# Optimization experiments

Measured on AMD Instinct MI355X. Metric: run time of the kernel, lower is better.

The kernel has to match this reference:

```python
import jax, jax.numpy as jnp
import numpy as np

C, HEADS, K, P, S = 384, 12, 3, 1, 1
B, H, W = 8, 56, 56


def _unfold(v, k, p, s):
    # v: [B, C, Hs, Ws] -> [B, C, k*k, oh*ow], matching torch.nn.Unfold layout
    b, c, hs, ws = v.shape
    vp = jnp.pad(v, ((0, 0), (0, 0), (p, p), (p, p)))
    oh = (hs + 2 * p - k) // s + 1
    ow = (ws + 2 * p - k) // s + 1
    patches = jnp.stack(
        [vp[:, :, i:i + oh * s:s, j:j + ow * s:s] for i in range(k) for j in range(k)],
        axis=2,
    )  # [B, C, k*k, oh, ow]
    return patches.reshape(b, c, k * k, oh * ow)


def _fold(patches, out_h, out_w, k, p, s):
    # patches: [B, C, k*k, oh, ow] -> scatter-add to [B, C, out_h, out_w]
    b, c, _, oh, ow = patches.shape
    out = jnp.zeros((b, c, out_h + 2 * p, out_w + 2 * p), patches.dtype)
    for i in range(k):
        for j in range(k):
            out = out.at[:, :, i:i + oh * s:s, j:j + ow * s:s].add(patches[:, :, i * k + j])
    return out[:, :, p:p + out_h, p:p + out_w]


def setup_inputs() -> dict:
    key = jax.random.key(0)
    ks = jax.random.split(key, 6)
    sc = C ** -0.5
    return {
        "x": jax.random.normal(ks[0], (B, C, H, W), jnp.float32),
        "Wv": jax.random.normal(ks[1], (C, C), jnp.float32) * sc,
        "Wa": jax.random.normal(ks[2], (K ** 4 * HEADS, C), jnp.float32) * sc,
        "ba": jax.random.normal(ks[3], (K ** 4 * HEADS,), jnp.float32) * 0.01,
        "Wp": jax.random.normal(ks[4], (C, C), jnp.float32) * sc,
        "bp": jax.random.normal(ks[5], (C,), jnp.float32) * 0.01,
    }


def reference(x, Wv, Wa, ba, Wp, bp):
    b, c, h, w = x.shape
    hd = c // HEADS
    height = -(-h // S)
    width = -(-w // S)
    L = height * width
    x_hwc = x.transpose(0, 2, 3, 1)  # [B,H,W,C]
    # value projection, then the original's spatial transpose quirk: [B,C,W,H]
    v = jnp.einsum('bhwc,dc->bdwh', x_hwc, Wv)
    v = _unfold(v, K, P, S)  # [B, C, k*k, L]
    v = v.reshape(b, HEADS, hd, K * K, L).transpose(0, 1, 4, 3, 2)  # [B,n,L,k2,hd]
    # avgPool with kernel=stride=1 is identity
    a = jnp.einsum('bhwc,ec->bhwe', x_hwc, Wa) + ba
    a = a.reshape(b, L, HEADS, K * K, K * K).transpose(0, 2, 1, 3, 4)
    a = jax.nn.softmax(a * (hd ** -0.5), axis=-1)  # [B,n,L,k2,k2]
    out = jnp.einsum('bnlpq,bnlqd->bnlpd', a, v)  # [B,n,L,k2,hd]
    out = out.transpose(0, 1, 4, 3, 2).reshape(b, c, K * K, height, width)
    out = _fold(out, h, w, K, P, S)  # [B,C,H,W]
    out = jnp.einsum('bchw,dc->bhwd', out, Wp) + bp
    return out.transpose(0, 3, 1, 2)
```

## Files before the change

kernel.cpp:

```cpp
#include <hip/hip_runtime.h>
#include <hip/hip_bf16.h>
#include <math.h>

#define BATCH 8
#define CIN   384
#define HEADS 12
#define HGT   56
#define WID   56
#define HW    3136
#define NPIX  (BATCH*HW)
#define NVAL  384
#define NATT_W 1152
#define NQKV  1536
#define KSTEPS (CIN/32)
#define MB_TOT 196

typedef __bf16 bf16x8 __attribute__((ext_vector_type(8)));
typedef __bf16 bf16x4 __attribute__((ext_vector_type(4)));
typedef float f32x4 __attribute__((ext_vector_type(4)));
typedef __hip_bfloat16 hbf16;

__device__ __forceinline__ void gload_lds16(const void* g, void* l) {
  __builtin_amdgcn_global_load_lds(
      (const __attribute__((address_space(1))) void*)g,
      (__attribute__((address_space(3))) void*)l, 16, 0, 0);
}

#define NB_CONVX 9408
#define NB_WQKV  2304
#define NB_WP    576
__global__ __launch_bounds__(256) void prep_all(
    const float* __restrict__ x,
    const float* __restrict__ Wv, const float* __restrict__ Wa,
    const float* __restrict__ ba, const float* __restrict__ Wp,
    hbf16* __restrict__ xb, hbf16* __restrict__ wcat,
    float* __restrict__ bcat, hbf16* __restrict__ wpb)
{
  const int bid = blockIdx.x;
  const int tid = threadIdx.x;
  if (bid < NB_CONVX) {
    __shared__ float s[32][33];
    const int xt = bid % 98;
    const int yt = (bid / 98) % 12;
    const int b  = bid / (98 * 12);
    const int hw0 = xt * 32, c0 = yt * 32;
    const int tx = tid & 31, ty = tid >> 5;
    #pragma unroll
    for (int i = 0; i < 4; i++) {
      int c = c0 + ty + i * 8;
      s[ty + i * 8][tx] = x[((size_t)b * CIN + c) * HW + hw0 + tx];
    }
    __syncthreads();
    #pragma unroll
    for (int i = 0; i < 4; i++) {
      int hw = hw0 + ty + i * 8;
      xb[((size_t)b * HW + hw) * CIN + c0 + tx] =
          __float2bfloat16(s[tx][ty + i * 8]);
    }
  } else if (bid < NB_CONVX + NB_WQKV) {
    const int i = (bid - NB_CONVX) * 256 + tid;
    if (i < NQKV * CIN) {
      int n = i / CIN, k = i % CIN;
      float v = 0.f;
      if (n < NVAL) {
        v = Wv[(size_t)n * CIN + k];
      } else {
        int a = n - NVAL;
        int head = a / 96, r = a % 96, p = r / 10, q = r % 10;
        if (p < 9 && q < 9)
          v = Wa[(size_t)(head * 81 + p * 9 + q) * CIN + k];
      }
      wcat[i] = __float2bfloat16(v);
    }
    if (i < NQKV) {
      float bv = 0.f;
      if (i >= NVAL) {
        int a = i - NVAL;
        int head = a / 96, r = a % 96, p = r / 10, q = r % 10;
        if (p < 9 && q < 9) bv = ba[head * 81 + p * 9 + q];
      }
      bcat[i] = bv;
    }
  } else {
    const int i = (bid - NB_CONVX - NB_WQKV) * 256 + tid;
    if (i < CIN * CIN) wpb[i] = __float2bfloat16(Wp[i]);
  }
}

template<int MODE>
__global__ __launch_bounds__(256, 4) void gemm_fused(
    const hbf16* __restrict__ A_,
    const hbf16* __restrict__ Bt_,
    const float* __restrict__ bias,
    hbf16* __restrict__ ovp,
    hbf16* __restrict__ oat,
    float* __restrict__ oput)
{
  __shared__ __align__(16) char smem[33280];
  const __bf16* A  = (const __bf16*)A_;
  const __bf16* Bt = (const __bf16*)Bt_;

  const int tid  = threadIdx.x;
  const int wave = tid >> 6, lane = tid & 63;
  const int wr = wave >> 1, wc = wave & 1;
  const int l16 = lane & 15, kg = lane >> 4;

  const int NBN   = (MODE == 0) ? (NQKV / 128) : (NVAL / 128);
  const int FULLB = 8 * NBN * (MB_TOT / 8);
  int mb, nb;
  {
    const int wgid = blockIdx.x;
    if (wgid < FULLB) {
      const int xc = wgid & 7, r = wgid >> 3;
      nb = r % NBN;
      mb = (r / NBN) * 8 + xc;
    } else {
      const int l = wgid - FULLB;
      nb = l >> 2;
      mb = (MB_TOT & ~7) + (l & 3);
    }
  }
  const int m0 = mb * 128, n0 = nb * 128;

  float* biasLds = (float*)(smem + 32768);
  if (tid < 128) biasLds[tid] = bias[n0 + tid];

  const int srow = tid >> 2;
  const int skb  = (tid & 3) * 16;

  f32x4 acc[4][4] = {};

  auto stage = [&](int k0, int buf) {
    const char* gA = (const char*)(A  + (size_t)m0 * CIN + k0);
    const char* gB = (const char*)(Bt + (size_t)n0 * CIN + k0);
    char* lA = smem + buf * 16384;
    char* lB = smem + buf * 16384 + 8192;
    #pragma unroll
    for (int p = 0; p < 2; p++) {
      int row = p * 64 + srow;
      gload_lds16(gA + (size_t)row * (CIN * 2) + skb, lA + p * 4096 + wave * 1024);
      gload_lds16(gB + (size_t)row * (CIN * 2) + skb, lB + p * 4096 + wave * 1024);
    }
  };

  stage(0, 0);
  __syncthreads();

  for (int t = 0; t < KSTEPS; ++t) {
    const int buf = t & 1;
    if (t + 1 < KSTEPS) stage((t + 1) * 32, buf ^ 1);

    const __bf16* As = (const __bf16*)(smem + buf * 16384);
    const __bf16* Bs = (const __bf16*)(smem + buf * 16384 + 8192);
    bf16x8 af[4], bfr[4];
    #pragma unroll
    for (int mi = 0; mi < 4; mi++)
      af[mi] = *(const bf16x8*)(As + (wr * 64 + mi * 16 + l16) * 32 + kg * 8);
    #pragma unroll
    for (int ni = 0; ni < 4; ni++)
      bfr[ni] = *(const bf16x8*)(Bs + (wc * 64 + ni * 16 + l16) * 32 + kg * 8);
    #pragma unroll
    for (int mi = 0; mi < 4; mi++)
      #pragma unroll
      for (int ni = 0; ni < 4; ni++) {
        if (MODE == 0)
          acc[ni][mi] = __builtin_amdgcn_mfma_f32_16x16x32_bf16(
              bfr[ni], af[mi], acc[ni][mi], 0, 0, 0);
        else
          acc[mi][ni] = __builtin_amdgcn_mfma_f32_16x16x32_bf16(
              af[mi], bfr[ni], acc[mi][ni], 0, 0, 0);
      }
    __syncthreads();
  }

  if (MODE == 0) {
    __bf16* epi = (__bf16*)smem;
    #pragma unroll
    for (int ni = 0; ni < 4; ni++) {
      #pragma unroll
      for (int mi = 0; mi < 4; mi++) {
        const int m  = wr * 64 + mi * 16 + l16;
        const int nb2 = wc * 64 + ni * 16 + kg * 4;
        bf16x4 v4;
        #pragma unroll
        for (int r = 0; r < 4; r++)
          v4[r] = (__bf16)__float2bfloat16(acc[ni][mi][r] + biasLds[nb2 + r]);
        *(bf16x4*)(epi + m * 128 + (nb2 ^ ((m & 7) << 3))) = v4;
      }
    }
    __syncthreads();
    const bool isv = (n0 < NVAL);
    #pragma unroll
    for (int q = 0; q < 8; q++) {
      const int cid = q * 256 + tid;
      const int m = cid >> 4, nc = cid & 15;
      const int nloc = nc * 8;
      bf16x8 v = *(const bf16x8*)(epi + m * 128 + (nloc ^ ((m & 7) << 3)));
      const int mg = m0 + m;
      if (isv)
        *(bf16x8*)(ovp + (size_t)mg * NVAL + n0 + nloc) = v;
      else
        *(bf16x8*)(oat + (size_t)mg * NATT_W + (n0 - NVAL) + nloc) = v;
    }
  } else {
    float* epi = (float*)smem;
    #pragma unroll
    for (int p = 0; p < 2; p++) {
      if (p) __syncthreads();
      if (wr == p) {
        #pragma unroll
        for (int mi = 0; mi < 4; mi++) {
          #pragma unroll
          for (int ni = 0; ni < 4; ni++) {
            const int n  = wc * 64 + ni * 16 + l16;
            const int ml = mi * 16 + kg * 4;
            f32x4 v;
            #pragma unroll
            for (int r = 0; r < 4; r++) v[r] = acc[mi][ni][r] + biasLds[n];
            *(f32x4*)(epi + n * 64 + (ml ^ ((n & 7) << 2))) = v;
          }
        }
      }
      __syncthreads();
      #pragma unroll
      for (int q = 0; q < 8; q++) {
        const int cid = q * 256 + tid;
        const int n = cid >> 4, mc = cid & 15;
        const int ml = mc * 4;
        f32x4 v = *(const f32x4*)(epi + n * 64 + (ml ^ ((n & 7) << 2)));
        const int mg = m0 + p * 64 + ml;
        const int b = mg / HW, hw = mg % HW;
        *(f32x4*)(oput + ((size_t)b * NVAL + n0 + n) * HW + hw) = v;
      }
    }
  }
}

__global__ __launch_bounds__(256) void fold_fused(
    const hbf16* __restrict__ attnb,
    const hbf16* __restrict__ vprojb,
    hbf16* __restrict__ foldedb)
{
  __shared__ float Wl[16 * HEADS * 25];

  const int b    = blockIdx.x & 7;
  const int tile = blockIdx.x >> 3;
  const int tx = tile % 14, ty = tile / 14;
  const int x0 = tx * 4, y0 = ty * 4;
  const int bofs = b * HW;
  const int tid = threadIdx.x;
  const bool interior = (tx >= 1) && (tx <= 12) && (ty >= 1) && (ty <= 12);
  const float scale = 0.17677669529663687f;

  if (tid < 192) {
    const int pixL = tid / HEADS, head = tid - pixL * HEADS;
    const int y = y0 + (pixL >> 2), x = x0 + (pixL & 3);

    float W[25];
    #pragma unroll
    for (int k = 0; k < 25; k++) W[k] = 0.f;

    auto docenter = [&](int i, int j) {
      const uint32_t* rp = (const uint32_t*)(attnb +
          (size_t)(bofs + (y - i + 1) * WID + (x - j + 1)) * NATT_W +
          head * 96 + (i * 3 + j) * 10);
      float v[9];
      #pragma unroll
      for (int u = 0; u < 4; u++) {
        uint32_t bits = rp[u];
        v[2 * u]     = __uint_as_float(bits << 16) * scale;
        v[2 * u + 1] = __uint_as_float(bits & 0xffff0000u) * scale;
      }
      v[8] = __uint_as_float(rp[4] << 16) * scale;
      float m = -1e30f;
      #pragma unroll
      for (int q = 0; q < 9; q++) m = fmaxf(m, v[q]);
      float s = 0.f;
      #pragma unroll
      for (int q = 0; q < 9; q++) { v[q] = __expf(v[q] - m); s += v[q]; }
      const float inv = 1.f / s;
      #pragma unroll
      for (int ip = 0; ip < 3; ip++)
        #pragma unroll
        for (int jp = 0; jp < 3; jp++)
          W[(ip - i + 2) * 5 + (jp - j + 2)] += v[ip * 3 + jp] * inv;
    };

    if (interior) {
      #pragma unroll
      for (int i = 0; i < 3; i++)
        #pragma unroll
        for (int j = 0; j < 3; j++)
          docenter(i, j);
    } else {
      #pragma unroll
      for (int i = 0; i < 3; i++)
        #pragma unroll
        for (int j = 0; j < 3; j++) {
          const int hh = y - i + 1, ww = x - j + 1;
          if (hh >= 0 && hh < HGT && ww >= 0 && ww < WID) docenter(i, j);
        }
    }
    float* o = &Wl[tid * 25];
    #pragma unroll
    for (int k = 0; k < 25; k++) o[k] = W[k];
  }
  __syncthreads();

  const int pixL = tid >> 4;
  const int ch16 = tid & 15;
  const int y = y0 + (pixL >> 2), x = x0 + (pixL & 3);
  const size_t pixofs = (size_t)(bofs + y * WID + x);
  const hbf16* vb0 = vprojb + (size_t)(bofs + (x - 2) * WID + (y - 2)) * NVAL;

  #pragma unroll
  for (int it = 0; it < 3; it++) {
    const int c0 = ch16 * 8 + it * 128;
    const int head = c0 >> 5;
    const float* Wp = &Wl[(pixL * HEADS + head) * 25];
    float acc[8];
    #pragma unroll
    for (int k = 0; k < 8; k++) acc[k] = 0.f;

    if (interior) {
      #pragma unroll
      for (int a = 0; a < 5; a++)
        #pragma unroll
        for (int e = 0; e < 5; e++) {
          const float w_ = Wp[a * 5 + e];
          const uint32_t* v = (const uint32_t*)(vb0 + (e * WID + a) * NVAL + c0);
          uint32_t b0 = v[0], b1 = v[1], b2 = v[2], b3 = v[3];
          acc[0] += w_ * __uint_as_float(b0 << 16);
          acc[1] += w_ * __uint_as_float(b0 & 0xffff0000u);
          acc[2] += w_ * __uint_as_float(b1 << 16);
          acc[3] += w_ * __uint_as_float(b1 & 0xffff0000u);
          acc[4] += w_ * __uint_as_float(b2 << 16);
          acc[5] += w_ * __uint_as_float(b2 & 0xffff0000u);
          acc[6] += w_ * __uint_as_float(b3 << 16);
          acc[7] += w_ * __uint_as_float(b3 & 0xffff0000u);
        }
    } else {
      #pragma unroll
      for (int a = 0; a < 5; a++) {
        const int wi = y + a - 2;
        #pragma unroll
        for (int e = 0; e < 5; e++) {
          const int hi = x + e - 2;
          if (wi >= 0 && wi < WID && hi >= 0 && hi < HGT) {
            const float w_ = Wp[a * 5 + e];
            const uint32_t* v = (const uint32_t*)(
                vprojb + (size_t)(bofs + hi * WID + wi) * NVAL + c0);
            uint32_t b0 = v[0], b1 = v[1], b2 = v[2], b3 = v[3];
            acc[0] += w_ * __uint_as_float(b0 << 16);
            acc[1] += w_ * __uint_as_float(b0 & 0xffff0000u);
            acc[2] += w_ * __uint_as_float(b1 << 16);
            acc[3] += w_ * __uint_as_float(b1 & 0xffff0000u);
            acc[4] += w_ * __uint_as_float(b2 << 16);
            acc[5] += w_ * __uint_as_float(b2 & 0xffff0000u);
            acc[6] += w_ * __uint_as_float(b3 << 16);
            acc[7] += w_ * __uint_as_float(b3 & 0xffff0000u);
          }
        }
      }
    }

    bf16x8 o;
    #pragma unroll
    for (int k = 0; k < 8; k++) o[k] = (__bf16)__float2bfloat16(acc[k]);
    *(bf16x8*)(foldedb + pixofs * NVAL + c0) = o;
  }
}

extern "C" void kernel_launch(void* const* d_in, const int* in_sizes, int n_in,
                              void* d_out, int out_size, void* d_ws, size_t ws_size,
                              hipStream_t stream)
{
  const float* x  = (const float*)d_in[0];
  const float* Wv = (const float*)d_in[1];
  const float* Wa = (const float*)d_in[2];
  const float* ba = (const float*)d_in[3];
  const float* Wp = (const float*)d_in[4];
  const float* bp = (const float*)d_in[5];
  float* out = (float*)d_out;

  char* w = (char*)d_ws;
  const size_t ATTN_B  = (size_t)NPIX * NATT_W * 2;
  const size_t VPROJ_B = (size_t)NPIX * NVAL * 2;
  const size_t XB_B    = (size_t)NPIX * CIN * 2;
  hbf16* attnb  = (hbf16*)w;
  hbf16* vprojb = (hbf16*)(w + ATTN_B);
  hbf16* xb     = (hbf16*)(w + ATTN_B + VPROJ_B);
  hbf16* wcat   = (hbf16*)(w + ATTN_B + VPROJ_B + XB_B);
  hbf16* wpb    = wcat + (size_t)NQKV * CIN;
  float* bcat   = (float*)(wpb + (size_t)CIN * CIN);
  hbf16* foldedb = xb;

  prep_all<<<dim3(NB_CONVX + NB_WQKV + NB_WP), 256, 0, stream>>>(
      x, Wv, Wa, ba, Wp, xb, wcat, bcat, wpb);
  gemm_fused<0><<<dim3(MB_TOT * (NQKV / 128)), 256, 0, stream>>>(
      xb, wcat, bcat, vprojb, attnb, nullptr);
  fold_fused<<<dim3(8 * 196), 256, 0, stream>>>(attnb, vprojb, foldedb);
  gemm_fused<1><<<dim3(MB_TOT * (NVAL / 128)), 256, 0, stream>>>(
      foldedb, wpb, bp, nullptr, nullptr, out);
}
```

Before: 121.6 us.

## Fuse softmax into attention GEMM epilogue and scatter normalized weights to centers

Splits the QKV GEMM into a value-projection GEMM and a separate per-head attention GEMM with 96-wide N tiles whose epilogue performs the 9-way softmax and writes normalized weights scattered to the neighbor-center pixel layout. The fold kernel then reads one contiguous 192-byte row per (pixel, head) instead of nine strided gathers, and no longer recomputes softmax for each of the nine overlapping neighbors. This removes the ninefold redundant exp/normalize work and the gather traffic in fold. In exchange it adds an extra kernel launch, N tiles with partial B loads (96 of 128 rows), uncoalesced 4-byte scattered stores in the attention epilogue, and a new block-to-tile mapping that launches some idle blocks.

Measured after the change: 143.3 us. +17.9%, slower.

```diff
diff --git a/kernel.cpp b/kernel.cpp
--- a/kernel.cpp
+++ b/kernel.cpp
@@ -11,13 +11,14 @@
 #define NPIX  (BATCH*HW)
 #define NVAL  384
 #define NATT_W 1152
-#define NQKV  1536
 #define KSTEPS (CIN/32)
 #define MB_TOT 196
+#define NQKV  1536
 
 typedef __bf16 bf16x8 __attribute__((ext_vector_type(8)));
 typedef __bf16 bf16x4 __attribute__((ext_vector_type(4)));
 typedef float f32x4 __attribute__((ext_vector_type(4)));
+typedef uint32_t u32x4 __attribute__((ext_vector_type(4)));
 typedef __hip_bfloat16 hbf16;
 
 __device__ __forceinline__ void gload_lds16(const void* g, void* l) {
@@ -93,9 +94,14 @@
     const hbf16* __restrict__ Bt_,
     const float* __restrict__ bias,
     hbf16* __restrict__ ovp,
-    hbf16* __restrict__ oat,
     float* __restrict__ oput)
 {
+  const int xcd = blockIdx.x & 7;
+  const int idx = blockIdx.x >> 3;
+  const int mb = xcd * 25 + idx / 3;
+  const int nb = idx % 3;
+  if (mb >= MB_TOT) return;
+
   __shared__ __align__(16) char smem[33280];
   const __bf16* A  = (const __bf16*)A_;
   const __bf16* Bt = (const __bf16*)Bt_;
@@ -104,22 +110,6 @@
   const int wave = tid >> 6, lane = tid & 63;
   const int wr = wave >> 1, wc = wave & 1;
   const int l16 = lane & 15, kg = lane >> 4;
-
-  const int NBN   = (MODE == 0) ? (NQKV / 128) : (NVAL / 128);
-  const int FULLB = 8 * NBN * (MB_TOT / 8);
-  int mb, nb;
-  {
-    const int wgid = blockIdx.x;
-    if (wgid < FULLB) {
-      const int xc = wgid & 7, r = wgid >> 3;
-      nb = r % NBN;
-      mb = (r / NBN) * 8 + xc;
-    } else {
-      const int l = wgid - FULLB;
-      nb = l >> 2;
-      mb = (MB_TOT & ~7) + (l & 3);
-    }
-  }
   const int m0 = mb * 128, n0 = nb * 128;
 
   float* biasLds = (float*)(smem + 32768);
@@ -189,18 +179,13 @@
       }
     }
     __syncthreads();
-    const bool isv = (n0 < NVAL);
     #pragma unroll
     for (int q = 0; q < 8; q++) {
       const int cid = q * 256 + tid;
       const int m = cid >> 4, nc = cid & 15;
       const int nloc = nc * 8;
       bf16x8 v = *(const bf16x8*)(epi + m * 128 + (nloc ^ ((m & 7) << 3)));
-      const int mg = m0 + m;
-      if (isv)
-        *(bf16x8*)(ovp + (size_t)mg * NVAL + n0 + nloc) = v;
-      else
-        *(bf16x8*)(oat + (size_t)mg * NATT_W + (n0 - NVAL) + nloc) = v;
+      *(bf16x8*)(ovp + (size_t)(m0 + m) * NVAL + n0 + nloc) = v;
     }
   } else {
     float* epi = (float*)smem;
@@ -236,8 +221,142 @@
   }
 }
 
+__global__ __launch_bounds__(256, 4) void gemm_attn(
+    const hbf16* __restrict__ A_,
+    const hbf16* __restrict__ Bt_,
+    const float* __restrict__ bias,
+    hbf16* __restrict__ attn2)
+{
+  const int xcd = blockIdx.x & 7;
+  const int idx = blockIdx.x >> 3;
+  const int mb = xcd * 25 + idx / 12;
+  const int h  = idx % 12;
+  if (mb >= MB_TOT) return;
+
+  __shared__ __align__(16) char smem[33280];
+  const __bf16* A  = (const __bf16*)A_;
+  const __bf16* Bt = (const __bf16*)Bt_;
+
+  const int tid  = threadIdx.x;
+  const int wave = tid >> 6, lane = tid & 63;
+  const int wr = wave >> 1, wc = wave & 1;
+  const int l16 = lane & 15, kg = lane >> 4;
+  const int m0 = mb * 128;
+  const int n0w = NVAL + h * 96;
+
+  float* biasLds = (float*)(smem + 32768);
+  if (tid < 96) biasLds[tid] = bias[n0w + tid];
+
+  const int srow = tid >> 2;
+  const int skb  = (tid & 3) * 16;
+
+  f32x4 acc[3][4] = {};
+
+  auto stage = [&](int k0, int buf) {
+    const char* gA = (const char*)(A  + (size_t)m0 * CIN + k0);
+    const char* gB = (const char*)(Bt + (size_t)n0w * CIN + k0);
+    char* lA = smem + buf * 16384;
+    char* lB = smem + buf * 16384 + 8192;
+    #pragma unroll
+    for (int p = 0; p < 2; p++) {
+      int row = p * 64 + srow;
+      gload_lds16(gA + (size_t)row * (CIN * 2) + skb, lA + p * 4096 + wave * 1024);
+      if (row < 96)
+        gload_lds16(gB + (size_t)row * (CIN * 2) + skb, lB + p * 4096 + wave * 1024);
+    }
+  };
+
+  stage(0, 0);
+  __syncthreads();
+
+  for (int t = 0; t < KSTEPS; ++t) {
+    const int buf = t & 1;
+    if (t + 1 < KSTEPS) stage((t + 1) * 32, buf ^ 1);
+
+    const __bf16* As = (const __bf16*)(smem + buf * 16384);
+    const __bf16* Bs = (const __bf16*)(smem + buf * 16384 + 8192);
+    bf16x8 af[4], bfr[3];
+    #pragma unroll
+    for (int mi = 0; mi < 4; mi++)
+      af[mi] = *(const bf16x8*)(As + (wr * 64 + mi * 16 + l16) * 32 + kg * 8);
+    #pragma unroll
+    for (int ni = 0; ni < 3; ni++)
+      bfr[ni] = *(const bf16x8*)(Bs + (wc * 48 + ni * 16 + l16) * 32 + kg * 8);
+    #pragma unroll
+    for (int mi = 0; mi < 4; mi++)
+      #pragma unroll
+      for (int ni = 0; ni < 3; ni++)
+        acc[ni][mi] = __builtin_amdgcn_mfma_f32_16x16x32_bf16(
+            bfr[ni], af[mi], acc[ni][mi], 0, 0, 0);
+    __syncthreads();
+  }
+
+  __bf16* epi = (__bf16*)smem;
+  #pragma unroll
+  for (int ni = 0; ni < 3; ni++) {
+    #pragma unroll
+    for (int mi = 0; mi < 4; mi++) {
+      const int m  = wr * 64 + mi * 16 + l16;
+      const int nbse = wc * 48 + ni * 16 + kg * 4;
+      bf16x4 v4;
+      #pragma unroll
+      for (int r = 0; r < 4; r++)
+        v4[r] = (__bf16)__float2bfloat16(acc[ni][mi][r] + biasLds[nbse + r]);
+      *(bf16x4*)(epi + m * 100 + nbse) = v4;
+    }
+  }
+  __syncthreads();
+
+  const float scale = 0.17677669529663687f;
+  #pragma unroll
+  for (int it = 0; it < 5; it++) {
+    const int u = it * 256 + tid;
+    if (u < 1152) {
+      const int m = u & 127, p = u >> 7;
+      const uint32_t* rp = (const uint32_t*)(epi + m * 100 + p * 10);
+      float v[9];
+      #pragma unroll
+      for (int t2 = 0; t2 < 4; t2++) {
+        uint32_t bits = rp[t2];
+        v[2 * t2]     = __uint_as_float(bits << 16) * scale;
+        v[2 * t2 + 1] = __uint_as_float(bits & 0xffff0000u) * scale;
+      }
+      v[8] = __uint_as_float(rp[4] << 16) * scale;
+      float mx = -1e30f;
+      #pragma unroll
+      for (int q = 0; q < 9; q++) mx = fmaxf(mx, v[q]);
+      float s = 0.f;
+      #pragma unroll
+      for (int q = 0; q < 9; q++) { v[q] = __expf(v[q] - mx); s += v[q]; }
+      const float inv = 1.f / s;
+      #pragma unroll
+      for (int q = 0; q < 9; q++) v[q] *= inv;
+
+      const int mg = m0 + m;
+      const int b = mg / HW, yx = mg % HW;
+      const int y = yx / WID, x = yx % WID;
+      const int i = p / 3, j = p % 3;
+      const int yC = y + i - 1, xC = x + j - 1;
+      if ((unsigned)yC < HGT && (unsigned)xC < WID) {
+        uint32_t* dst = (uint32_t*)(attn2 +
+            (size_t)(b * HW + yC * WID + xC) * NATT_W + h * 96 + p * 10);
+        union { __bf16 hh[2]; uint32_t u32; } pk;
+        #pragma unroll
+        for (int k = 0; k < 4; k++) {
+          pk.hh[0] = (__bf16)__float2bfloat16(v[2 * k]);
+          pk.hh[1] = (__bf16)__float2bfloat16(v[2 * k + 1]);
+          dst[k] = pk.u32;
+        }
+        pk.hh[0] = (__bf16)__float2bfloat16(v[8]);
+        pk.hh[1] = (__bf16)0.f;
+        dst[4] = pk.u32;
+      }
+    }
+  }
+}
+
 __global__ __launch_bounds__(256) void fold_fused(
-    const hbf16* __restrict__ attnb,
+    const hbf16* __restrict__ attn2,
     const hbf16* __restrict__ vprojb,
     hbf16* __restrict__ foldedb)
 {
@@ -250,56 +369,45 @@
   const int bofs = b * HW;
   const int tid = threadIdx.x;
   const bool interior = (tx >= 1) && (tx <= 12) && (ty >= 1) && (ty <= 12);
-  const float scale = 0.17677669529663687f;
 
   if (tid < 192) {
     const int pixL = tid / HEADS, head = tid - pixL * HEADS;
     const int y = y0 + (pixL >> 2), x = x0 + (pixL & 3);
 
+    const u32x4* base = (const u32x4*)(attn2 +
+        (size_t)(bofs + y * WID + x) * NATT_W + head * 96);
+    u32x4 dv[12];
+    #pragma unroll
+    for (int k = 0; k < 12; k++) dv[k] = base[k];
+
     float W[25];
     #pragma unroll
     for (int k = 0; k < 25; k++) W[k] = 0.f;
 
-    auto docenter = [&](int i, int j) {
-      const uint32_t* rp = (const uint32_t*)(attnb +
-          (size_t)(bofs + (y - i + 1) * WID + (x - j + 1)) * NATT_W +
-          head * 96 + (i * 3 + j) * 10);
+    #pragma unroll
+    for (int r = 0; r < 9; r++) {
+      const int i = r / 3, j = r % 3;
+      if (!interior) {
+        const int hh = y - i + 1, ww = x - j + 1;
+        if (!((unsigned)hh < HGT && (unsigned)ww < WID)) continue;
+      }
       float v[9];
       #pragma unroll
-      for (int u = 0; u < 4; u++) {
-        uint32_t bits = rp[u];
-        v[2 * u]     = __uint_as_float(bits << 16) * scale;
-        v[2 * u + 1] = __uint_as_float(bits & 0xffff0000u) * scale;
-      }
-      v[8] = __uint_as_float(rp[4] << 16) * scale;
-      float m = -1e30f;
-      #pragma unroll
-      for (int q = 0; q < 9; q++) m = fmaxf(m, v[q]);
-      float s = 0.f;
-      #pragma unroll
-      for (int q = 0; q < 9; q++) { v[q] = __expf(v[q] - m); s += v[q]; }
-      const float inv = 1.f / s;
+      for (int t = 0; t < 4; t++) {
+        const int k = 5 * r + t;
+        const uint32_t bits = dv[k >> 2][k & 3];
+        v[2 * t]     = __uint_as_float(bits << 16);
+        v[2 * t + 1] = __uint_as_float(bits & 0xffff0000u);
+      }
+      {
+        const int k = 5 * r + 4;
+        v[8] = __uint_as_float(dv[k >> 2][k & 3] << 16);
+      }
       #pragma unroll
       for (int ip = 0; ip < 3; ip++)
         #pragma unroll
         for (int jp = 0; jp < 3; jp++)
-          W[(ip - i + 2) * 5 + (jp - j + 2)] += v[ip * 3 + jp] * inv;
-    };
-
-    if (interior) {
-      #pragma unroll
-      for (int i = 0; i < 3; i++)
-        #pragma unroll
-        for (int j = 0; j < 3; j++)
-          docenter(i, j);
-    } else {
-      #pragma unroll
-      for (int i = 0; i < 3; i++)
-        #pragma unroll
-        for (int j = 0; j < 3; j++) {
-          const int hh = y - i + 1, ww = x - j + 1;
-          if (hh >= 0 && hh < HGT && ww >= 0 && ww < WID) docenter(i, j);
-        }
+          W[(ip - i + 2) * 5 + (jp - j + 2)] += v[ip * 3 + jp];
     }
     float* o = &Wl[tid * 25];
     #pragma unroll
@@ -387,7 +495,7 @@
   const size_t ATTN_B  = (size_t)NPIX * NATT_W * 2;
   const size_t VPROJ_B = (size_t)NPIX * NVAL * 2;
   const size_t XB_B    = (size_t)NPIX * CIN * 2;
-  hbf16* attnb  = (hbf16*)w;
+  hbf16* attn2  = (hbf16*)w;
   hbf16* vprojb = (hbf16*)(w + ATTN_B);
   hbf16* xb     = (hbf16*)(w + ATTN_B + VPROJ_B);
   hbf16* wcat   = (hbf16*)(w + ATTN_B + VPROJ_B + XB_B);
@@ -397,9 +505,8 @@
 
   prep_all<<<dim3(NB_CONVX + NB_WQKV + NB_WP), 256, 0, stream>>>(
       x, Wv, Wa, ba, Wp, xb, wcat, bcat, wpb);
-  gemm_fused<0><<<dim3(MB_TOT * (NQKV / 128)), 256, 0, stream>>>(
-      xb, wcat, bcat, vprojb, attnb, nullptr);
-  fold_fused<<<dim3(8 * 196), 256, 0, stream>>>(attnb, vprojb, foldedb);
-  gemm_fused<1><<<dim3(MB_TOT * (NVAL / 128)), 256, 0, stream>>>(
-      foldedb, wpb, bp, nullptr, nullptr, out);
+  gemm_fused<0><<<dim3(600), 256, 0, stream>>>(xb, wcat, bcat, vprojb, nullptr);
+  gemm_attn<<<dim3(2400), 256, 0, stream>>>(xb, wcat, bcat, attn2);
+  fold_fused<<<dim3(8 * 196), 256, 0, stream>>>(attn2, vprojb, foldedb);
+  gemm_fused<1><<<dim3(600), 256, 0, stream>>>(foldedb, wpb, bp, nullptr, out);
 }
```
